# Kernel optimization log

Hardware: AMD Instinct MI355X
Metric: run time of the kernel (lower is better)

Reference implementation:

```python
import jax, jax.numpy as jnp
from jax import lax
import numpy as np

B, T, I = 1024, 128, 128   # batch, seq_len, input_dim
H = 256                     # n_z (GRU hidden)
K = 8                       # n_clusters
E1, E2, C = 512, 256, 2     # expert MLP widths, n_classes
ALPHA = 1.0


def _glorot(key, shape, scale=0.05):
    return jax.random.normal(key, shape, dtype=jnp.float32) * scale


def setup_inputs() -> dict:
    key = jax.random.key(0)
    ks = jax.random.split(key, 16)
    inp = {
        "x": jax.random.normal(ks[0], (B, T, I), dtype=jnp.float32),
        # GRU encoder layer 0: input I -> hidden H (PyTorch gate order r,z,n)
        "W_ih0": _glorot(ks[1], (3 * H, I)),
        "W_hh0": _glorot(ks[2], (3 * H, H)),
        "b_ih0": jnp.zeros((3 * H,), jnp.float32),
        "b_hh0": jnp.zeros((3 * H,), jnp.float32),
        # GRU encoder layer 1: input H -> hidden H
        "W_ih1": _glorot(ks[3], (3 * H, H)),
        "W_hh1": _glorot(ks[4], (3 * H, H)),
        "b_ih1": jnp.zeros((3 * H,), jnp.float32),
        "b_hh1": jnp.zeros((3 * H,), jnp.float32),
        # soft-cluster centers [K, H]
        "cluster_centers": _glorot(ks[5], (K, H), scale=1.0),
        # stacked per-cluster expert MLP params (grouped GEMM form)
        "eW1": _glorot(ks[6], (K, E1, H)),
        "eb1": jnp.zeros((K, E1), jnp.float32),
        "eW2": _glorot(ks[7], (K, E2, E1)),
        "eb2": jnp.zeros((K, E2), jnp.float32),
        "eW3": _glorot(ks[8], (K, C, E2)),
        "eb3": jnp.zeros((K, C), jnp.float32),
    }
    return inp


def gru_layer(x_tbi, W_ih, W_hh, b_ih, b_hh):
    """PyTorch-compatible GRU layer. x_tbi: [T, B, in]. Returns [T, B, H]."""
    Hh = W_hh.shape[1]
    h0 = jnp.zeros((x_tbi.shape[1], Hh), x_tbi.dtype)

    def step(h, xt):
        gi = xt @ W_ih.T + b_ih          # [B, 3H]
        gh = h @ W_hh.T + b_hh           # [B, 3H]
        ir, iz, in_ = jnp.split(gi, 3, axis=-1)
        hr, hz, hn = jnp.split(gh, 3, axis=-1)
        r = jax.nn.sigmoid(ir + hr)
        z = jax.nn.sigmoid(iz + hz)
        n = jnp.tanh(in_ + r * hn)
        h_new = (1.0 - z) * n + z * h
        return h_new, h_new

    _, ys = lax.scan(step, h0, x_tbi)
    return ys


def reference(x, W_ih0, W_hh0, b_ih0, b_hh0, W_ih1, W_hh1, b_ih1, b_hh1,
              cluster_centers, eW1, eb1, eW2, eb2, eW3, eb3):
    # --- 2-layer GRU encoder ---
    xt = jnp.transpose(x, (1, 0, 2))                      # [T, B, I]
    h_l0 = gru_layer(xt, W_ih0, W_hh0, b_ih0, b_hh0)      # [T, B, H]
    h_l1 = gru_layer(h_l0, W_ih1, W_hh1, b_ih1, b_hh1)    # [T, B, H]
    z = h_l1[-1]                                          # [B, H] last-step latent

    # --- soft cluster assignment q (Student-t, alpha=1) ---
    d2 = jnp.sum((z[:, None, :] - cluster_centers[None]) ** 2, axis=-1)  # [B, K]
    q = (1.0 / (1.0 + d2 / ALPHA)) ** ((ALPHA + 1.0) / 2.0)
    q = q / jnp.sum(q, axis=1, keepdims=True)             # [B, K]

    # --- all experts on all latents (attention=True path), grouped GEMMs ---
    h1 = jax.nn.relu(jnp.einsum('bh,keh->bke', z, eW1) + eb1)    # [B, K, E1]
    h2 = jax.nn.relu(jnp.einsum('bke,kfe->bkf', h1, eW2) + eb2)  # [B, K, E2]
    logits = jnp.einsum('bkf,kcf->bkc', h2, eW3) + eb3           # [B, K, C]

    # --- q-weighted combine: preds[:,c] = sum_k q[:,k] * logits[:,k,c] ---
    preds = jnp.einsum('bk,bkc->bc', q, logits)                  # [B, C]
    return preds
```

## Files before the change

### kernel.cpp

```cpp
#include <hip/hip_runtime.h>
#include <math.h>


template<int ACT>
__global__ __launch_bounds__(256)
void gemm_f32(const float* __restrict__ A, const float* __restrict__ W,
              const float* __restrict__ bias, float* __restrict__ C,
              int K,
              long a_sT, long a_sB, long a_sZ,
              long w_sZ, long b_sZ, long c_row, long c_sZ)
{
  __shared__ alignas(16) float As[16][132];
  __shared__ alignas(16) float Ws[16][132];
  const int z = blockIdx.z;
  const float* Az = A + (long)z * a_sZ;
  const float* Wz = W + (long)z * w_sZ;
  const float* bz = bias + (long)z * b_sZ;
  const int m0 = blockIdx.y * 128;
  const int n0 = blockIdx.x * 128;
  const int tid = threadIdx.x;
  const int tx = tid & 15, ty = tid >> 4;

  const int row0 = tid >> 2, kq0 = tid & 3;
  const int row1 = (tid + 256) >> 2, kq1 = kq0;

  float acc[8][8];
  #pragma unroll
  for (int i = 0; i < 8; ++i)
    #pragma unroll
    for (int j = 0; j < 8; ++j) acc[i][j] = 0.f;

  const int ma0 = m0 + row0, ma1 = m0 + row1;
  const float* apr0 = Az + (long)(ma0 >> 10) * a_sT + (long)(ma0 & 1023) * a_sB + kq0 * 4;
  const float* apr1 = Az + (long)(ma1 >> 10) * a_sT + (long)(ma1 & 1023) * a_sB + kq1 * 4;
  const float* wpr0 = Wz + (long)(n0 + row0) * K + kq0 * 4;
  const float* wpr1 = Wz + (long)(n0 + row1) * K + kq1 * 4;

  float4 pa0 = *(const float4*)(apr0);
  float4 pa1 = *(const float4*)(apr1);
  float4 pw0 = *(const float4*)(wpr0);
  float4 pw1 = *(const float4*)(wpr1);

  for (int k0 = 0; k0 < K; k0 += 16) {
    As[kq0*4+0][row0] = pa0.x; As[kq0*4+1][row0] = pa0.y;
    As[kq0*4+2][row0] = pa0.z; As[kq0*4+3][row0] = pa0.w;
    As[kq1*4+0][row1] = pa1.x; As[kq1*4+1][row1] = pa1.y;
    As[kq1*4+2][row1] = pa1.z; As[kq1*4+3][row1] = pa1.w;
    Ws[kq0*4+0][row0] = pw0.x; Ws[kq0*4+1][row0] = pw0.y;
    Ws[kq0*4+2][row0] = pw0.z; Ws[kq0*4+3][row0] = pw0.w;
    Ws[kq1*4+0][row1] = pw1.x; Ws[kq1*4+1][row1] = pw1.y;
    Ws[kq1*4+2][row1] = pw1.z; Ws[kq1*4+3][row1] = pw1.w;
    __syncthreads();

    if (k0 + 16 < K) {
      pa0 = *(const float4*)(apr0 + k0 + 16);
      pa1 = *(const float4*)(apr1 + k0 + 16);
      pw0 = *(const float4*)(wpr0 + k0 + 16);
      pw1 = *(const float4*)(wpr1 + k0 + 16);
    }

    #pragma unroll
    for (int kk = 0; kk < 16; ++kk) {
      float4 a0 = *(const float4*)&As[kk][ty * 8];
      float4 a1 = *(const float4*)&As[kk][ty * 8 + 4];
      float4 b0 = *(const float4*)&Ws[kk][tx * 4];
      float4 b1 = *(const float4*)&Ws[kk][64 + tx * 4];
      float a[8] = {a0.x,a0.y,a0.z,a0.w,a1.x,a1.y,a1.z,a1.w};
      float b[8] = {b0.x,b0.y,b0.z,b0.w,b1.x,b1.y,b1.z,b1.w};
      #pragma unroll
      for (int i = 0; i < 8; ++i)
        #pragma unroll
        for (int j = 0; j < 8; ++j)
          acc[i][j] = fmaf(a[i], b[j], acc[i][j]);
    }
    __syncthreads();
  }

  float4 bv0 = *(const float4*)&bz[n0 + tx * 4];
  float4 bv1 = *(const float4*)&bz[n0 + 64 + tx * 4];
  #pragma unroll
  for (int i = 0; i < 8; ++i) {
    int m = m0 + ty * 8 + i;
    float* cp = C + (long)m * c_row + (long)z * c_sZ + n0;
    float4 o0, o1;
    o0.x = acc[i][0] + bv0.x; o0.y = acc[i][1] + bv0.y;
    o0.z = acc[i][2] + bv0.z; o0.w = acc[i][3] + bv0.w;
    o1.x = acc[i][4] + bv1.x; o1.y = acc[i][5] + bv1.y;
    o1.z = acc[i][6] + bv1.z; o1.w = acc[i][7] + bv1.w;
    if (ACT == 1) {
      o0.x = fmaxf(o0.x, 0.f); o0.y = fmaxf(o0.y, 0.f);
      o0.z = fmaxf(o0.z, 0.f); o0.w = fmaxf(o0.w, 0.f);
      o1.x = fmaxf(o1.x, 0.f); o1.y = fmaxf(o1.y, 0.f);
      o1.z = fmaxf(o1.z, 0.f); o1.w = fmaxf(o1.w, 0.f);
    }
    *(float4*)(cp + tx * 4) = o0;
    *(float4*)(cp + 64 + tx * 4) = o1;
  }
}

__global__ __launch_bounds__(64)
void transpose_whh(const float* __restrict__ W, float4* __restrict__ Wt)
{
  const int row = blockIdx.x;
  const int k4 = threadIdx.x;
  const int g = row >> 8, d = row & 255;
  float4 v = *(const float4*)(W + (long)row * 256 + k4 * 4);
  Wt[((long)k4 * 3 + g) * 256 + d] = v;
}

__global__ __launch_bounds__(1024)
void gru_rec(const float* __restrict__ gi, const float4* __restrict__ Wt,
             const float* __restrict__ b_hh, float* __restrict__ h_state,
             float* __restrict__ h_out, int Tc, int store_all)
{
  __shared__ alignas(16) float hs[4][256];
  __shared__ float part[4][12][256];
  const int tid = threadIdx.x;
  const int d = tid & 255;
  const int q = tid >> 8;
  const int b0 = blockIdx.x * 4;
  hs[q][d] = h_state[(long)(b0 + q) * 256 + d];
  __syncthreads();

  const float bhr = b_hh[d];
  const float bhz = b_hh[256 + d];
  const float bhn = b_hh[512 + d];
  const int k4lo = q * 16;
  const float4* Wp = Wt + d;

  for (int t = 0; t < Tc; ++t) {
    const float* gip = gi + ((long)t * 1024 + b0 + q) * 768;
    const float gir = gip[d];
    const float giz = gip[256 + d];
    const float gin = gip[512 + d];

    float ar[4] = {0,0,0,0}, az[4] = {0,0,0,0}, an[4] = {0,0,0,0};
    #pragma unroll 8
    for (int k4i = 0; k4i < 16; ++k4i) {
      const int k4 = k4lo + k4i;
      float4 wr = Wp[(k4 * 3 + 0) * 256];
      float4 wz = Wp[(k4 * 3 + 1) * 256];
      float4 wn = Wp[(k4 * 3 + 2) * 256];
      #pragma unroll
      for (int r = 0; r < 4; ++r) {
        float4 hv = *(const float4*)&hs[r][k4 * 4];
        ar[r] = fmaf(hv.x, wr.x, ar[r]); ar[r] = fmaf(hv.y, wr.y, ar[r]);
        ar[r] = fmaf(hv.z, wr.z, ar[r]); ar[r] = fmaf(hv.w, wr.w, ar[r]);
        az[r] = fmaf(hv.x, wz.x, az[r]); az[r] = fmaf(hv.y, wz.y, az[r]);
        az[r] = fmaf(hv.z, wz.z, az[r]); az[r] = fmaf(hv.w, wz.w, az[r]);
        an[r] = fmaf(hv.x, wn.x, an[r]); an[r] = fmaf(hv.y, wn.y, an[r]);
        an[r] = fmaf(hv.z, wn.z, an[r]); an[r] = fmaf(hv.w, wn.w, an[r]);
      }
    }
    #pragma unroll
    for (int r = 0; r < 4; ++r) {
      part[q][0 * 4 + r][d] = ar[r];
      part[q][1 * 4 + r][d] = az[r];
      part[q][2 * 4 + r][d] = an[r];
    }
    __syncthreads();

    {
      float sr = ar[q], sz = az[q], sn = an[q];
      #pragma unroll
      for (int qq = 0; qq < 4; ++qq) {
        if (qq == q) continue;
        sr += part[qq][0 * 4 + q][d];
        sz += part[qq][1 * 4 + q][d];
        sn += part[qq][2 * 4 + q][d];
      }
      float rg = 1.f / (1.f + __expf(-(gir + sr + bhr)));
      float zg = 1.f / (1.f + __expf(-(giz + sz + bhz)));
      float ng = tanhf(gin + rg * (sn + bhn));
      float hn = (1.f - zg) * ng + zg * hs[q][d];
      hs[q][d] = hn;
      if (store_all)
        h_out[((long)t * 1024 + b0 + q) * 256 + d] = hn;
    }
    __syncthreads();
  }
  h_state[(long)(b0 + q) * 256 + d] = hs[q][d];
}

__global__ __launch_bounds__(64)
void cluster_q(const float* __restrict__ zlat, const float* __restrict__ centers,
               float* __restrict__ q)
{
  __shared__ float red[64];
  __shared__ float qv[8];
  const int b = blockIdx.x;
  const int tid = threadIdx.x;
  const int k = tid >> 3, p = tid & 7;
  const float4* zp = (const float4*)(zlat + (long)b * 256 + p * 32);
  const float4* cp = (const float4*)(centers + (long)k * 256 + p * 32);
  float s = 0.f;
  #pragma unroll
  for (int i = 0; i < 8; ++i) {
    float4 zv = zp[i], cv = cp[i];
    float dx = zv.x - cv.x, dy = zv.y - cv.y;
    float dz = zv.z - cv.z, dw = zv.w - cv.w;
    s += dx*dx + dy*dy + dz*dz + dw*dw;
  }
  red[tid] = s;
  __syncthreads();
  if (tid < 8) {
    float d2 = 0.f;
    #pragma unroll
    for (int p2 = 0; p2 < 8; ++p2) d2 += red[tid * 8 + p2];
    qv[tid] = 1.f / (1.f + d2);
  }
  __syncthreads();
  if (tid < 8) {
    float ssum = 0.f;
    #pragma unroll
    for (int kk = 0; kk < 8; ++kk) ssum += qv[kk];
    q[(long)b * 8 + tid] = qv[tid] / ssum;
  }
}

__global__ __launch_bounds__(256)
void combine_preds(const float* __restrict__ h2, const float* __restrict__ eW3,
                   const float* __restrict__ eb3, const float* __restrict__ q,
                   float* __restrict__ out)
{
  __shared__ float p0[256], p1[256];
  __shared__ float lc[16];
  const int b = blockIdx.x;
  const int tid = threadIdx.x;
  const int k = tid >> 5, w = tid & 31;
  const float* h2p = h2 + (long)b * (8 * 256) + (long)k * 256 + w * 8;
  const float* w0  = eW3 + (long)k * 512 + w * 8;
  const float* w1  = eW3 + (long)k * 512 + 256 + w * 8;
  float c0 = 0.f, c1 = 0.f;
  #pragma unroll
  for (int i = 0; i < 8; ++i) {
    float hv = h2p[i];
    c0 = fmaf(hv, w0[i], c0);
    c1 = fmaf(hv, w1[i], c1);
  }
  p0[tid] = c0; p1[tid] = c1;
  __syncthreads();
  if (tid < 16) {
    int kk = tid >> 1, c = tid & 1;
    const float* pp = (c == 0) ? p0 : p1;
    float s = 0.f;
    for (int w2 = 0; w2 < 32; ++w2) s += pp[kk * 32 + w2];
    s += eb3[kk * 2 + c];
    lc[tid] = q[(long)b * 8 + kk] * s;
  }
  __syncthreads();
  if (tid < 2) {
    float s = 0.f;
    #pragma unroll
    for (int kk = 0; kk < 8; ++kk) s += lc[kk * 2 + tid];
    out[(long)b * 2 + tid] = s;
  }
}

__global__ __launch_bounds__(256)
void zero_fill(float* __restrict__ p, long n)
{
  long i = (long)blockIdx.x * 256 + threadIdx.x;
  if (i < n) p[i] = 0.f;
}

extern "C" void kernel_launch(void* const* d_in, const int* in_sizes, int n_in,
                              void* d_out, int out_size, void* d_ws, size_t ws_size,
                              hipStream_t stream)
{
  const float* x       = (const float*)d_in[0];
  const float* W_ih0   = (const float*)d_in[1];
  const float* W_hh0   = (const float*)d_in[2];
  const float* b_ih0   = (const float*)d_in[3];
  const float* b_hh0   = (const float*)d_in[4];
  const float* W_ih1   = (const float*)d_in[5];
  const float* W_hh1   = (const float*)d_in[6];
  const float* b_ih1   = (const float*)d_in[7];
  const float* b_hh1   = (const float*)d_in[8];
  const float* centers = (const float*)d_in[9];
  const float* eW1     = (const float*)d_in[10];
  const float* eb1     = (const float*)d_in[11];
  const float* eW2     = (const float*)d_in[12];
  const float* eb2     = (const float*)d_in[13];
  const float* eW3     = (const float*)d_in[14];
  const float* eb3     = (const float*)d_in[15];
  float* out = (float*)d_out;
  (void)in_sizes; (void)n_in; (void)out_size;

  char* base = (char*)d_ws;
  size_t off = 0;
  auto alloc = [&](size_t nbytes) -> void* {
    void* p = base + off;
    off += (nbytes + 255) & ~(size_t)255;
    return p;
  };
  float* h0_state = (float*)alloc(1024ull * 256 * 4);
  float* h1_state = (float*)alloc(1024ull * 256 * 4);
  float* qbuf     = (float*)alloc(1024ull * 8 * 4);
  float* h1buf    = (float*)alloc(1024ull * 8 * 512 * 4);
  float* h2buf    = (float*)alloc(1024ull * 8 * 256 * 4);
  float4* Wt0     = (float4*)alloc(768ull * 256 * 4);
  float4* Wt1     = (float4*)alloc(768ull * 256 * 4);
  const size_t fixed = off;

  int Tc = 2;
  const int cands[7] = {128, 64, 32, 16, 8, 4, 2};
  for (int ci = 0; ci < 7; ++ci) {
    size_t need = fixed + (size_t)cands[ci] * 1024 * (768 + 768 + 256) * 4 + 1024;
    if (need <= ws_size) { Tc = cands[ci]; break; }
  }
  float* gi0 = (float*)alloc((size_t)Tc * 1024 * 768 * 4);
  float* gi1 = (float*)alloc((size_t)Tc * 1024 * 768 * 4);
  float* h0c = (float*)alloc((size_t)Tc * 1024 * 256 * 4);

  {
    long n = 2L * 1024 * 256;
    zero_fill<<<dim3((unsigned)((n + 255) / 256)), 256, 0, stream>>>(h0_state, n);
    transpose_whh<<<768, 64, 0, stream>>>(W_hh0, Wt0);
    transpose_whh<<<768, 64, 0, stream>>>(W_hh1, Wt1);
  }

  for (int t0 = 0; t0 < 128; t0 += Tc) {
    gemm_f32<0><<<dim3(6, Tc * 8, 1), 256, 0, stream>>>(
        x + (long)t0 * 128, W_ih0, b_ih0, gi0, 128,
         128,  128L * 128,  0,
         0,  0,  768,  0);
    gru_rec<<<256, 1024, 0, stream>>>(gi0, Wt0, b_hh0, h0_state, h0c, Tc, 1);

    gemm_f32<0><<<dim3(6, Tc * 8, 1), 256, 0, stream>>>(
        h0c, W_ih1, b_ih1, gi1, 256,
         1024L * 256,  256,  0,
         0,  0,  768,  0);
    gru_rec<<<256, 1024, 0, stream>>>(gi1, Wt1, b_hh1, h1_state, nullptr, Tc, 0);
  }

  cluster_q<<<1024, 64, 0, stream>>>(h1_state, centers, qbuf);

  gemm_f32<1><<<dim3(4, 8, 8), 256, 0, stream>>>(
      h1_state, eW1, eb1, h1buf, 256,
       0,  256,  0,
       512L * 256,  512,  8L * 512,  512);
  gemm_f32<1><<<dim3(2, 8, 8), 256, 0, stream>>>(
      h1buf, eW2, eb2, h2buf, 512,
       0,  8L * 512,  512,
       256L * 512,  256,  8L * 256,  256);

  combine_preds<<<1024, 256, 0, stream>>>(h2buf, eW3, eb3, qbuf, out);
}
```

Measured before the change: 3.323 ms.

## Overlap GRU layer-1 chunk with layer-0 next chunk in one dual kernel

The recurrent GRU body moves into a shared device function, and a new dual kernel is added. It launches 512 blocks: the first half runs layer 1 on chunk c and the second half runs layer 0 on chunk c+1. This wavefront schedule lets the two independent recurrences fill the GPU together, so the two layers no longer serialize for every time chunk. The launch bounds also gain a min-blocks hint. That hint may cap registers and cause spills in the unrolled recurrence.

```diff
diff --git a/kernel.cpp b/kernel.cpp
--- a/kernel.cpp
+++ b/kernel.cpp
@@ -108,17 +108,16 @@
   Wt[((long)k4 * 3 + g) * 256 + d] = v;
 }
 
-__global__ __launch_bounds__(1024)
-void gru_rec(const float* __restrict__ gi, const float4* __restrict__ Wt,
-             const float* __restrict__ b_hh, float* __restrict__ h_state,
-             float* __restrict__ h_out, int Tc, int store_all)
-{
-  __shared__ alignas(16) float hs[4][256];
-  __shared__ float part[4][12][256];
+__device__ __forceinline__
+void gru_body(const float* __restrict__ gi, const float4* __restrict__ Wt,
+              const float* __restrict__ b_hh, float* __restrict__ h_state,
+              float* __restrict__ h_out, int Tc, int store_all,
+              int blk, float (*hs)[256], float (*part)[12][256])
+{
   const int tid = threadIdx.x;
   const int d = tid & 255;
   const int q = tid >> 8;
-  const int b0 = blockIdx.x * 4;
+  const int b0 = blk * 4;
   hs[q][d] = h_state[(long)(b0 + q) * 256 + d];
   __syncthreads();
 
@@ -180,6 +179,34 @@
     __syncthreads();
   }
   h_state[(long)(b0 + q) * 256 + d] = hs[q][d];
+}
+
+__global__ __launch_bounds__(1024, 8)
+void gru_rec(const float* __restrict__ gi, const float4* __restrict__ Wt,
+             const float* __restrict__ b_hh, float* __restrict__ h_state,
+             float* __restrict__ h_out, int Tc, int store_all)
+{
+  __shared__ alignas(16) float hs[4][256];
+  __shared__ float part[4][12][256];
+  gru_body(gi, Wt, b_hh, h_state, h_out, Tc, store_all, blockIdx.x, hs, part);
+}
+
+__global__ __launch_bounds__(1024, 8)
+void gru_dual(const float* __restrict__ giA, const float4* __restrict__ WtA,
+              const float* __restrict__ bA, float* __restrict__ hA,
+              float* __restrict__ hoA, int stA,
+              const float* __restrict__ giB, const float4* __restrict__ WtB,
+              const float* __restrict__ bB, float* __restrict__ hB,
+              float* __restrict__ hoB, int stB, int Tc)
+{
+  __shared__ alignas(16) float hs[4][256];
+  __shared__ float part[4][12][256];
+  const int bid = blockIdx.x;
+  if (bid < 256) {
+    gru_body(giA, WtA, bA, hA, hoA, Tc, stA, bid, hs, part);
+  } else {
+    gru_body(giB, WtB, bB, hB, hoB, Tc, stB, bid - 256, hs, part);
+  }
 }
 
 __global__ __launch_bounds__(64)
@@ -312,6 +339,7 @@
   float* gi0 = (float*)alloc((size_t)Tc * 1024 * 768 * 4);
   float* gi1 = (float*)alloc((size_t)Tc * 1024 * 768 * 4);
   float* h0c = (float*)alloc((size_t)Tc * 1024 * 256 * 4);
+  const int N = 128 / Tc;
 
   {
     long n = 2L * 1024 * 256;
@@ -320,19 +348,31 @@
     transpose_whh<<<768, 64, 0, stream>>>(W_hh1, Wt1);
   }
 
-  for (int t0 = 0; t0 < 128; t0 += Tc) {
+  auto launch_gemm0 = [&](int c) {
     gemm_f32<0><<<dim3(6, Tc * 8, 1), 256, 0, stream>>>(
-        x + (long)t0 * 128, W_ih0, b_ih0, gi0, 128,
+        x + (long)c * Tc * 128, W_ih0, b_ih0, gi0, 128,
          128,  128L * 128,  0,
          0,  0,  768,  0);
-    gru_rec<<<256, 1024, 0, stream>>>(gi0, Wt0, b_hh0, h0_state, h0c, Tc, 1);
-
+  };
+  auto launch_gemm1 = [&]() {
     gemm_f32<0><<<dim3(6, Tc * 8, 1), 256, 0, stream>>>(
         h0c, W_ih1, b_ih1, gi1, 256,
          1024L * 256,  256,  0,
          0,  0,  768,  0);
-    gru_rec<<<256, 1024, 0, stream>>>(gi1, Wt1, b_hh1, h1_state, nullptr, Tc, 0);
-  }
+  };
+
+  launch_gemm0(0);
+  gru_rec<<<256, 1024, 0, stream>>>(gi0, Wt0, b_hh0, h0_state, h0c, Tc, 1);
+  for (int c = 0; c < N - 1; ++c) {
+    launch_gemm1();
+    launch_gemm0(c + 1);
+    gru_dual<<<512, 1024, 0, stream>>>(
+        gi1, Wt1, b_hh1, h1_state, nullptr, 0,
+        gi0, Wt0, b_hh0, h0_state, h0c, 1,
+        Tc);
+  }
+  launch_gemm1();
+  gru_rec<<<256, 1024, 0, stream>>>(gi1, Wt1, b_hh1, h1_state, nullptr, Tc, 0);
 
   cluster_q<<<1024, 64, 0, stream>>>(h1_state, centers, qbuf);
 
```

Result: slower. 3.744 ms (+12.7%).
